# Kernel tuning notes

Hardware: AMD Instinct MI355X
Metric: run time of the kernel (lower is better)

The kernel has to match this reference:

```python
import jax, jax.numpy as jnp
import numpy as np

N_SOTU, N_TAXON = 100000, 20000
E, EL = 800000, 200000
D_S, D_T, H = 256, 128, 256


def setup_inputs() -> dict:
    key = jax.random.key(0)
    ks = jax.random.split(key, 32)
    nrm = lambda k, shp: jax.random.normal(k, shp, jnp.float32) * 0.05
    inp = {}
    inp["x_sotu"] = nrm(ks[0], (N_SOTU, D_S))
    inp["x_taxon"] = nrm(ks[1], (N_TAXON, D_T))
    inp["edge_src"] = jax.random.randint(ks[2], (E,), 0, N_SOTU)   # sotu end
    inp["edge_dst"] = jax.random.randint(ks[3], (E,), 0, N_TAXON)  # taxon end
    inp["label_src"] = jax.random.randint(ks[4], (EL,), 0, N_SOTU)
    inp["label_dst"] = jax.random.randint(ks[5], (EL,), 0, N_TAXON)
    # conv1, edge type sotu->taxon
    inp["Wl1_st"] = nrm(ks[6], (H, D_S)); inp["bl1_st"] = jnp.zeros((H,), jnp.float32)
    inp["Wr1_st"] = nrm(ks[7], (H, D_T))
    # conv1, edge type taxon->sotu (reverse)
    inp["Wl1_ts"] = nrm(ks[8], (H, D_T)); inp["bl1_ts"] = jnp.zeros((H,), jnp.float32)
    inp["Wr1_ts"] = nrm(ks[9], (H, D_S))
    # conv2 (hidden -> hidden) per edge type
    inp["Wl2_st"] = nrm(ks[10], (H, H)); inp["bl2_st"] = jnp.zeros((H,), jnp.float32)
    inp["Wr2_st"] = nrm(ks[11], (H, H))
    inp["Wl2_ts"] = nrm(ks[12], (H, H)); inp["bl2_ts"] = jnp.zeros((H,), jnp.float32)
    inp["Wr2_ts"] = nrm(ks[13], (H, H))
    # final per-node-type linear (to_hetero duplicates Linear per node type)
    inp["Wlin_s"] = nrm(ks[14], (H, H)); inp["blin_s"] = jnp.zeros((H,), jnp.float32)
    inp["Wlin_t"] = nrm(ks[15], (H, H)); inp["blin_t"] = jnp.zeros((H,), jnp.float32)
    # edge decoder MLP
    inp["Wd1"] = nrm(ks[16], (H, 2 * H)); inp["bd1"] = jnp.zeros((H,), jnp.float32)
    inp["Wd2"] = nrm(ks[17], (1, H));     inp["bd2"] = jnp.zeros((1,), jnp.float32)
    return inp


def _sage(x_src, x_dst, src, dst, Wl, bl, Wr):
    """PyG SAGEConv (mean aggr): lin_l(mean of neighbor src feats) + lin_r(x_dst)."""
    n_dst = x_dst.shape[0]
    msum = jax.ops.segment_sum(x_src[src], dst, num_segments=n_dst)
    cnt = jax.ops.segment_sum(jnp.ones(src.shape, x_src.dtype), dst, num_segments=n_dst)
    m = msum / jnp.maximum(cnt, 1.0)[:, None]
    return m @ Wl.T + bl + x_dst @ Wr.T


def reference(x_sotu, x_taxon, edge_src, edge_dst, label_src, label_dst,
              Wl1_st, bl1_st, Wr1_st, Wl1_ts, bl1_ts, Wr1_ts,
              Wl2_st, bl2_st, Wr2_st, Wl2_ts, bl2_ts, Wr2_ts,
              Wlin_s, blin_s, Wlin_t, blin_t, Wd1, bd1, Wd2, bd2):
    # layer 1 (hetero SAGE, aggr='sum' over single incoming edge type per node type)
    h1_t = jax.nn.relu(_sage(x_sotu, x_taxon, edge_src, edge_dst, Wl1_st, bl1_st, Wr1_st))
    h1_s = jax.nn.relu(_sage(x_taxon, x_sotu, edge_dst, edge_src, Wl1_ts, bl1_ts, Wr1_ts))
    # layer 2
    h2_t = jax.nn.relu(_sage(h1_s, h1_t, edge_src, edge_dst, Wl2_st, bl2_st, Wr2_st))
    h2_s = jax.nn.relu(_sage(h1_t, h1_s, edge_dst, edge_src, Wl2_ts, bl2_ts, Wr2_ts))
    # per-node-type output projection
    z_s = h2_s @ Wlin_s.T + blin_s
    z_t = h2_t @ Wlin_t.T + blin_t
    # edge decoder: gather endpoint embeddings, concat, 2-layer MLP
    z = jnp.concatenate([z_s[label_src], z_t[label_dst]], axis=-1)  # [EL, 2H]
    h = jax.nn.relu(z @ Wd1.T + bd1)
    return (h @ Wd2.T + bd2).reshape(-1)  # [EL]
```

## Files before the change

### kernel.cpp

```cpp
#include <hip/hip_runtime.h>


constexpr int NS = 100000, NT = 20000;
constexpr int E_EDGES = 800000, EL_EDGES = 200000;
constexpr int DS = 256, DT = 128, H = 256;

constexpr int NB_T = 79, SH_T = 8, VB_T = 17;
constexpr int NB_S = 98, SH_S = 10, VB_S = 15;
constexpr int BIN_CAP = 96, CHUNK = 2048;
constexpr int CVT_BLOCKS = 2048;

typedef __attribute__((ext_vector_type(8))) short short8;
typedef __attribute__((ext_vector_type(4))) float float4v;
typedef __attribute__((ext_vector_type(8))) _Float16 half8v;
typedef unsigned short ushort_t;

__device__ __forceinline__ float bf2f(unsigned int u) {
    union { unsigned int i; float f; } x; x.i = u << 16; return x.f;
}
__device__ __forceinline__ unsigned short f2bf(float f) {
    union { float f; unsigned int i; } x; x.f = f;
    unsigned int r = x.i + 0x7FFFu + ((x.i >> 16) & 1u);
    return (unsigned short)(r >> 16);
}


struct GemmJob {
    const ushort_t* A1; const ushort_t* W1; int K1;
    const ushort_t* A2; const ushort_t* W2; int K2;
    const ushort_t* Add; const float* bias;
    void* C; int M; int flags;
};

struct GatherJob {
    const ushort_t* X; const int* rowptr; const int* cnt; const int* col;
    ushort_t* out; int N;
};

struct Gather128Job {
    const ushort_t* X; const int* rowptr; const int* cnt; const int* col;
    ushort_t* out; int N;
};

__device__ __forceinline__ void gemm_body(const GemmJob& jb, int bid)
{
    __shared__ ushort_t As[64][40];
    __shared__ ushort_t Bs[128][40];
    const int tid = threadIdx.x;
    const int M = jb.M;

    const int nx = (M + 63) >> 6;
    const int nx8 = nx & ~7;
    int rowblk, colblk;
    if (bid < nx8 * 2) {
        const int group = bid >> 4;
        const int xcd = bid & 7;
        const int half = (bid >> 3) & 1;
        rowblk = group * 8 + xcd;
        colblk = half;
    } else {
        const int r = bid - nx8 * 2;
        rowblk = nx8 + (r >> 1);
        colblk = r & 1;
    }
    const int row0 = rowblk * 64, col0 = colblk * 128;

    const int wave = tid >> 6, lane = tid & 63;
    const int wrow = (wave >> 1) * 32;
    const int wcol = (wave & 1) * 64;
    const int m16 = lane & 15, quad = lane >> 4;
    const int sr = tid >> 2;
    const int skc = (tid & 3) * 8;

    float4v acc[2][4];
#pragma unroll
    for (int i = 0; i < 2; i++)
#pragma unroll
        for (int j = 0; j < 4; j++) acc[i][j] = (float4v){0.f, 0.f, 0.f, 0.f};

#pragma unroll 1
    for (int pass = 0; pass < 2; pass++) {
        const ushort_t* A = pass ? jb.A2 : jb.A1;
        const ushort_t* W = pass ? jb.W2 : jb.W1;
        const int K = pass ? jb.K2 : jb.K1;
        if (!A) break;
        const int gra = row0 + sr;
        const bool oka = gra < M;
        const ushort_t* Ap = A + (size_t)gra * K + skc;
        const ushort_t* Wp0 = W + (size_t)(col0 + sr) * K + skc;
        const ushort_t* Wp1 = W + (size_t)(col0 + 64 + sr) * K + skc;

        uint4 a0 = make_uint4(0, 0, 0, 0);
        if (oka) a0 = *(const uint4*)Ap;
        uint4 b0 = *(const uint4*)Wp0;
        uint4 b1 = *(const uint4*)Wp1;

        for (int k0 = 0; k0 < K; k0 += 32) {
            __syncthreads();
            *(uint4*)&As[sr][skc] = a0;
            *(uint4*)&Bs[sr][skc] = b0;
            *(uint4*)&Bs[64 + sr][skc] = b1;
            __syncthreads();
            if (k0 + 32 < K) {
                a0 = make_uint4(0, 0, 0, 0);
                if (oka) a0 = *(const uint4*)(Ap + k0 + 32);
                b0 = *(const uint4*)(Wp0 + k0 + 32);
                b1 = *(const uint4*)(Wp1 + k0 + 32);
            }
            short8 af[2], bf[4];
#pragma unroll
            for (int i = 0; i < 2; i++)
                af[i] = *(const short8*)&As[wrow + i * 16 + m16][quad * 8];
#pragma unroll
            for (int j = 0; j < 4; j++)
                bf[j] = *(const short8*)&Bs[wcol + j * 16 + m16][quad * 8];
#pragma unroll
            for (int i = 0; i < 2; i++)
#pragma unroll
                for (int j = 0; j < 4; j++)
                    acc[i][j] = __builtin_amdgcn_mfma_f32_16x16x32_bf16(
                        af[i], bf[j], acc[i][j], 0, 0, 0);
        }
    }

    const bool relu = jb.flags & 1, f16out = jb.flags & 2;
#pragma unroll
    for (int i = 0; i < 2; i++) {
        const int rbase = row0 + wrow + i * 16 + quad * 4;
#pragma unroll
        for (int r = 0; r < 4; r++) {
            const int row = rbase + r;
            if (row >= M) continue;
#pragma unroll
            for (int j = 0; j < 4; j++) {
                const int col = col0 + wcol + j * 16 + m16;
                float v = acc[i][j][r];
                if (jb.Add) v += bf2f((unsigned int)jb.Add[(size_t)row * 256 + col]);
                if (jb.bias) v += jb.bias[col];
                if (relu) v = fmaxf(v, 0.f);
                if (f16out) ((_Float16*)jb.C)[(size_t)row * 256 + col] = (_Float16)v;
                else ((ushort_t*)jb.C)[(size_t)row * 256 + col] = f2bf(v);
            }
        }
    }
}

#define UNPACK_ADD(acc, v) \
    acc[0] += bf2f(v.x & 0xffff); acc[1] += bf2f(v.x >> 16); \
    acc[2] += bf2f(v.y & 0xffff); acc[3] += bf2f(v.y >> 16); \
    acc[4] += bf2f(v.z & 0xffff); acc[5] += bf2f(v.z >> 16); \
    acc[6] += bf2f(v.w & 0xffff); acc[7] += bf2f(v.w >> 16);

__device__ __forceinline__ void gather_body(const GatherJob& g, int gb)
{
    const int node = gb * 16 + (threadIdx.x >> 5);
    const int c = (threadIdx.x & 31) * 8;
    if (node >= g.N) return;
    const int beg = g.rowptr[node];
    const int deg = g.cnt[node];
    const int end = beg + deg;
    const ushort_t* __restrict__ X = g.X;
    const int* __restrict__ col = g.col;
    float a[8] = {0, 0, 0, 0, 0, 0, 0, 0};
    float b[8] = {0, 0, 0, 0, 0, 0, 0, 0};
    int i = beg;
    for (; i + 3 < end; i += 4) {
        const int c0 = col[i], c1 = col[i + 1], c2 = col[i + 2], c3 = col[i + 3];
        uint4 v0 = *(const uint4*)&X[(size_t)c0 * 256 + c];
        uint4 v1 = *(const uint4*)&X[(size_t)c1 * 256 + c];
        uint4 v2 = *(const uint4*)&X[(size_t)c2 * 256 + c];
        uint4 v3 = *(const uint4*)&X[(size_t)c3 * 256 + c];
        UNPACK_ADD(a, v0) UNPACK_ADD(b, v1) UNPACK_ADD(a, v2) UNPACK_ADD(b, v3)
    }
    for (; i + 1 < end; i += 2) {
        uint4 v0 = *(const uint4*)&X[(size_t)col[i] * 256 + c];
        uint4 v1 = *(const uint4*)&X[(size_t)col[i + 1] * 256 + c];
        UNPACK_ADD(a, v0) UNPACK_ADD(b, v1)
    }
    if (i < end) {
        uint4 v0 = *(const uint4*)&X[(size_t)col[i] * 256 + c];
        UNPACK_ADD(a, v0)
    }
    float inv = 1.f / fmaxf((float)deg, 1.f);
    uint4 o;
    o.x = (unsigned int)f2bf((a[0] + b[0]) * inv) | ((unsigned int)f2bf((a[1] + b[1]) * inv) << 16);
    o.y = (unsigned int)f2bf((a[2] + b[2]) * inv) | ((unsigned int)f2bf((a[3] + b[3]) * inv) << 16);
    o.z = (unsigned int)f2bf((a[4] + b[4]) * inv) | ((unsigned int)f2bf((a[5] + b[5]) * inv) << 16);
    o.w = (unsigned int)f2bf((a[6] + b[6]) * inv) | ((unsigned int)f2bf((a[7] + b[7]) * inv) << 16);
    *(uint4*)&g.out[(size_t)node * 256 + c] = o;
}

__device__ __forceinline__ void gather128_body(const Gather128Job& g, int gb)
{
    const int node = gb * 32 + (threadIdx.x >> 4);
    const int c = (threadIdx.x & 15) * 8;
    if (node >= g.N) return;
    const int beg = g.rowptr[node];
    const int deg = g.cnt[node];
    const int end = beg + deg;
    const ushort_t* __restrict__ X = g.X;
    const int* __restrict__ col = g.col;
    float a[8] = {0, 0, 0, 0, 0, 0, 0, 0};
    float b[8] = {0, 0, 0, 0, 0, 0, 0, 0};
    int i = beg;
    for (; i + 3 < end; i += 4) {
        const int c0 = col[i], c1 = col[i + 1], c2 = col[i + 2], c3 = col[i + 3];
        uint4 v0 = *(const uint4*)&X[(size_t)c0 * 128 + c];
        uint4 v1 = *(const uint4*)&X[(size_t)c1 * 128 + c];
        uint4 v2 = *(const uint4*)&X[(size_t)c2 * 128 + c];
        uint4 v3 = *(const uint4*)&X[(size_t)c3 * 128 + c];
        UNPACK_ADD(a, v0) UNPACK_ADD(b, v1) UNPACK_ADD(a, v2) UNPACK_ADD(b, v3)
    }
    for (; i + 1 < end; i += 2) {
        uint4 v0 = *(const uint4*)&X[(size_t)col[i] * 128 + c];
        uint4 v1 = *(const uint4*)&X[(size_t)col[i + 1] * 128 + c];
        UNPACK_ADD(a, v0) UNPACK_ADD(b, v1)
    }
    if (i < end) {
        uint4 v0 = *(const uint4*)&X[(size_t)col[i] * 128 + c];
        UNPACK_ADD(a, v0)
    }
    float inv = 1.f / fmaxf((float)deg, 1.f);
    uint4 o;
    o.x = (unsigned int)f2bf((a[0] + b[0]) * inv) | ((unsigned int)f2bf((a[1] + b[1]) * inv) << 16);
    o.y = (unsigned int)f2bf((a[2] + b[2]) * inv) | ((unsigned int)f2bf((a[3] + b[3]) * inv) << 16);
    o.z = (unsigned int)f2bf((a[4] + b[4]) * inv) | ((unsigned int)f2bf((a[5] + b[5]) * inv) << 16);
    o.w = (unsigned int)f2bf((a[6] + b[6]) * inv) | ((unsigned int)f2bf((a[7] + b[7]) * inv) << 16);
    *(uint4*)&g.out[(size_t)node * 128 + c] = o;
}

__device__ __forceinline__ void binA_body(
    const int* __restrict__ key, const int* __restrict__ val, int E,
    int nbins, int shift, int vbits,
    int* __restrict__ gcur, unsigned* __restrict__ stg, int ablk)
{
    __shared__ unsigned bins[NB_S * BIN_CAP];
    __shared__ int lcnt[NB_S], gbase[NB_S];
    const int tid = threadIdx.x;
    const int base = ablk * CHUNK;
    for (int i = tid; i < nbins; i += 256) lcnt[i] = 0;
    __syncthreads();
    const unsigned lowmask = (1u << shift) - 1u;
#pragma unroll
    for (int k = 0; k < CHUNK / 256; k++) {
        int e = base + k * 256 + tid;
        if (e < E) {
            int kk = key[e];
            int b = kk >> shift;
            unsigned pk = (((unsigned)kk & lowmask) << vbits) | (unsigned)val[e];
            int c = atomicAdd(&lcnt[b], 1);
            if (c < BIN_CAP) bins[b * BIN_CAP + c] = pk;
            else { int p = atomicAdd(&gcur[b], 1); stg[p] = pk; }
        }
    }
    __syncthreads();
    if (tid < nbins) gbase[tid] = atomicAdd(&gcur[tid], min(lcnt[tid], BIN_CAP));
    __syncthreads();
    for (int b = 0; b < nbins; b++) {
        int c = min(lcnt[b], BIN_CAP);
        for (int i = tid; i < c; i += 256) stg[gbase[b] + i] = bins[b * BIN_CAP + i];
    }
}

__device__ __forceinline__ void binB_body(
    const unsigned* __restrict__ stg, const int* __restrict__ rowptr,
    int N, int node_per, int vbits, int* __restrict__ colout, int bblk)
{
    __shared__ int cur[1024];
    const int tid = threadIdx.x;
    const int node0 = bblk * node_per;
    const int nn = min(node_per, N - node0);
    for (int i = tid; i < nn; i += 256) cur[i] = rowptr[node0 + i];
    const int estart = rowptr[node0];
    const int eend = rowptr[node0 + nn];
    __syncthreads();
    const unsigned vmask = (1u << vbits) - 1u;
    for (int i = estart + tid; i < eend; i += 256) {
        unsigned v = stg[i];
        int kl = (int)(v >> vbits);
        int pos = atomicAdd(&cur[kl], 1);
        colout[pos] = (int)(v & vmask);
    }
}

struct CvtJobs {
    const float* src[14];
    ushort_t* dst[14];
    int n4[14];
    int cnt;
};

__device__ __forceinline__ void cvt_body(const CvtJobs& jb, int nchunks,
                                         int ch0, int stride)
{
    const int t = threadIdx.x;
#pragma unroll 1
    for (int ch = ch0; ch < nchunks; ch += stride) {
        int idx = ch << 10;
        int k = 0;
        while (idx >= jb.n4[k]) { idx -= jb.n4[k]; ++k; }
        const float4* __restrict__ s = (const float4*)jb.src[k];
        ushort_t* __restrict__ d = jb.dst[k];
        const int base = idx + t;
        float4 v0 = s[base];
        float4 v1 = s[base + 256];
        float4 v2 = s[base + 512];
        float4 v3 = s[base + 768];
        uint2 o0, o1, o2, o3;
        o0.x = (unsigned int)f2bf(v0.x) | ((unsigned int)f2bf(v0.y) << 16);
        o0.y = (unsigned int)f2bf(v0.z) | ((unsigned int)f2bf(v0.w) << 16);
        o1.x = (unsigned int)f2bf(v1.x) | ((unsigned int)f2bf(v1.y) << 16);
        o1.y = (unsigned int)f2bf(v1.z) | ((unsigned int)f2bf(v1.w) << 16);
        o2.x = (unsigned int)f2bf(v2.x) | ((unsigned int)f2bf(v2.y) << 16);
        o2.y = (unsigned int)f2bf(v2.z) | ((unsigned int)f2bf(v2.w) << 16);
        o3.x = (unsigned int)f2bf(v3.x) | ((unsigned int)f2bf(v3.y) << 16);
        o3.y = (unsigned int)f2bf(v3.z) | ((unsigned int)f2bf(v3.w) << 16);
        *(uint2*)(d + (size_t)base * 4) = o0;
        *(uint2*)(d + (size_t)(base + 256) * 4) = o1;
        *(uint2*)(d + (size_t)(base + 512) * 4) = o2;
        *(uint2*)(d + (size_t)(base + 768) * 4) = o3;
    }
}

__device__ __forceinline__ void fold_body(
    const float* __restrict__ Wd1, const float* __restrict__ bd1,
    const float* __restrict__ Wlin_s, const float* __restrict__ blin_s,
    const float* __restrict__ Wlin_t, const float* __restrict__ blin_t,
    float* __restrict__ Wc_s, float* __restrict__ Wc_t,
    float* __restrict__ bu, float* __restrict__ bv, int b)
{
    const int t = threadIdx.x;
    if (b < 256) {
        float s = 0.f;
        for (int k = 0; k < 256; k++) s += Wd1[b * 512 + k] * Wlin_s[k * 256 + t];
        Wc_s[b * 256 + t] = s;
    } else if (b < 512) {
        const int h = b - 256;
        float s = 0.f;
        for (int k = 0; k < 256; k++) s += Wd1[h * 512 + 256 + k] * Wlin_t[k * 256 + t];
        Wc_t[h * 256 + t] = s;
    } else {
        float su = 0.f, sv = 0.f;
        for (int k = 0; k < 256; k++) {
            su += Wd1[t * 512 + k] * blin_s[k];
            sv += Wd1[t * 512 + 256 + k] * blin_t[k];
        }
        bu[t] = bd1[t] + su;
        bv[t] = sv;
    }
}

__device__ __forceinline__ void count_body(
    const int* __restrict__ src, const int* __restrict__ dst,
    int* __restrict__ cnt_s, int* __restrict__ cnt_t, int E, int cblk)
{
    const int base = cblk * 1024 + threadIdx.x;
    const int e0 = base, e1 = base + 256, e2 = base + 512, e3 = base + 768;
    int s0 = 0, s1 = 0, s2 = 0, s3 = 0;
    int d0 = 0, d1 = 0, d2 = 0, d3 = 0;
    if (e0 < E) { s0 = src[e0]; d0 = dst[e0]; }
    if (e1 < E) { s1 = src[e1]; d1 = dst[e1]; }
    if (e2 < E) { s2 = src[e2]; d2 = dst[e2]; }
    if (e3 < E) { s3 = src[e3]; d3 = dst[e3]; }
    if (e0 < E) { atomicAdd(&cnt_s[s0], 1); atomicAdd(&cnt_t[d0], 1); }
    if (e1 < E) { atomicAdd(&cnt_s[s1], 1); atomicAdd(&cnt_t[d1], 1); }
    if (e2 < E) { atomicAdd(&cnt_s[s2], 1); atomicAdd(&cnt_t[d2], 1); }
    if (e3 < E) { atomicAdd(&cnt_s[s3], 1); atomicAdd(&cnt_t[d3], 1); }
}

__global__ __launch_bounds__(256) void gemm_gemm_kernel(GemmJob a, int ablocks,
                                                        GemmJob b)
{
    const int bid = blockIdx.x;
    if (bid < ablocks) gemm_body(a, bid);
    else gemm_body(b, bid - ablocks);
}

__global__ __launch_bounds__(512) void gather_g128_kernel(GatherJob a, int ablocks,
                                                          Gather128Job b)
{
    const int bid = blockIdx.x;
    if (bid < ablocks) gather_body(a, bid);
    else gather128_body(b, bid - ablocks);
}

__global__ __launch_bounds__(512) void gather_gather_kernel(GatherJob a, int ablocks,
                                                            GatherJob b)
{
    const int bid = blockIdx.x;
    if (bid < ablocks) gather_body(a, bid);
    else gather_body(b, bid - ablocks);
}

__global__ __launch_bounds__(256) void fold_count_kernel(
    const float* Wd1, const float* bd1,
    const float* Wlin_s, const float* blin_s,
    const float* Wlin_t, const float* blin_t,
    float* Wc_s, float* Wc_t, float* bu, float* bv,
    const int* src, const int* dst, int* cnt_s, int* cnt_t, int E)
{
    const int bid = blockIdx.x;
    if (bid < 513)
        fold_body(Wd1, bd1, Wlin_s, blin_s, Wlin_t, blin_t, Wc_s, Wc_t, bu, bv, bid);
    else
        count_body(src, dst, cnt_s, cnt_t, E, bid - 513);
}

__global__ __launch_bounds__(256) void cvt_binA_kernel(
    CvtJobs jb, int nchunks, int aBlocks,
    const int* key, const int* val, int E, int nbins, int shift, int vbits,
    int* gcur, unsigned* stg)
{
    const int bid = blockIdx.x;
    if (bid < aBlocks)
        binA_body(key, val, E, nbins, shift, vbits, gcur, stg, bid);
    else
        cvt_body(jb, nchunks, bid - aBlocks, gridDim.x - aBlocks);
}

__global__ __launch_bounds__(256) void binA_binB_kernel(
    const int* keyA, const int* valA, int E, int nbinsA, int shiftA, int vbitsA,
    int* gcurA, unsigned* stgA, int aBlocks,
    const unsigned* stgB, const int* rowptrB, int NB, int nodeperB, int vbitsB,
    int* coloutB)
{
    const int bid = blockIdx.x;
    if (bid < aBlocks)
        binA_body(keyA, valA, E, nbinsA, shiftA, vbitsA, gcurA, stgA, bid);
    else
        binB_body(stgB, rowptrB, NB, nodeperB, vbitsB, coloutB, bid - aBlocks);
}

__global__ __launch_bounds__(256) void binB_kernel(
    const unsigned* __restrict__ stg, const int* __restrict__ rowptr,
    int N, int node_per, int vbits, int* __restrict__ colout)
{
    binB_body(stg, rowptr, N, node_per, vbits, colout, blockIdx.x);
}

__global__ __launch_bounds__(256) void psum_kernel(
    const int* __restrict__ cnt_s, const int* __restrict__ cnt_t,
    int* __restrict__ bsum_s, int* __restrict__ bsum_t, int nbS)
{
    const bool isS = (int)blockIdx.x < nbS;
    const int blk = isS ? blockIdx.x : blockIdx.x - nbS;
    const int N = isS ? NS : NT;
    const int* cnt = isS ? cnt_s : cnt_t;
    int* bsum = isS ? bsum_s : bsum_t;
    __shared__ int sdata[256];
    const int t = threadIdx.x;
    const int base = blk * 1024;
    int s = 0;
    for (int i = t; i < 1024; i += 256) {
        int idx = base + i;
        s += (idx < N) ? cnt[idx] : 0;
    }
    sdata[t] = s; __syncthreads();
    for (int off = 128; off > 0; off >>= 1) {
        if (t < off) sdata[t] += sdata[t + off];
        __syncthreads();
    }
    if (t == 0) bsum[blk] = sdata[0];
}

__global__ void sbsum_kernel(int* __restrict__ bsum_s, int* __restrict__ bsum_t,
                             int nbS, int nbT)
{
    if (threadIdx.x != 0) return;
    int* b = blockIdx.x ? bsum_t : bsum_s;
    int nb = blockIdx.x ? nbT : nbS;
    int run = 0;
    for (int i = 0; i < nb; i++) { int v = b[i]; b[i] = run; run += v; }
}

__global__ __launch_bounds__(256) void sblock_kernel(
    const int* __restrict__ cnt_s, const int* __restrict__ cnt_t,
    const int* __restrict__ bsum_s, const int* __restrict__ bsum_t,
    int* __restrict__ rowptr_s, int* __restrict__ rowptr_t, int nbS)
{
    const bool isS = (int)blockIdx.x < nbS;
    const int blk = isS ? blockIdx.x : blockIdx.x - nbS;
    const int N = isS ? NS : NT;
    const int* cnt = isS ? cnt_s : cnt_t;
    const int* bsum = isS ? bsum_s : bsum_t;
    int* rowptr = isS ? rowptr_s : rowptr_t;
    __shared__ int sc[256];
    const int t = threadIdx.x;
    const int base = blk * 1024 + t * 4;
    int v[4]; int s = 0;
#pragma unroll
    for (int j = 0; j < 4; j++) {
        int idx = base + j;
        v[j] = (idx < N) ? cnt[idx] : 0;
        s += v[j];
    }
    sc[t] = s; __syncthreads();
    for (int off = 1; off < 256; off <<= 1) {
        int add = (t >= off) ? sc[t - off] : 0;
        __syncthreads();
        sc[t] += add;
        __syncthreads();
    }
    int excl = sc[t] - s + bsum[blk];
#pragma unroll
    for (int j = 0; j < 4; j++) {
        int idx = base + j;
        if (idx < N) rowptr[idx] = excl;
        if (idx == N - 1) rowptr[N] = excl + v[j];
        excl += v[j];
    }
}

__global__ void binit_kernel(const int* __restrict__ rowptr_t,
                             const int* __restrict__ rowptr_s,
                             int* __restrict__ gcur_t, int* __restrict__ gcur_s)
{
    int t = threadIdx.x;
    if (t < NB_T) gcur_t[t] = rowptr_t[t << SH_T];
    if (t < NB_S) gcur_s[t] = rowptr_s[t << SH_S];
}

__global__ __launch_bounds__(256) void edge_score_kernel(
    const _Float16* __restrict__ U, const _Float16* __restrict__ V,
    const int* __restrict__ ls, const int* __restrict__ ld,
    const float* __restrict__ Wd2, const float* __restrict__ bd2,
    float* __restrict__ out, int EL)
{
    const int l32 = threadIdx.x & 31;
    const int e = blockIdx.x * 8 + (threadIdx.x >> 5);
    if (e >= EL) return;
    const int c = l32 * 8;
    half8v u = *(const half8v*)&U[(size_t)ls[e] * 256 + c];
    half8v v = *(const half8v*)&V[(size_t)ld[e] * 256 + c];
    float4 w0 = *(const float4*)&Wd2[c];
    float4 w1 = *(const float4*)&Wd2[c + 4];
    float s = fmaxf((float)u[0] + (float)v[0], 0.f) * w0.x
            + fmaxf((float)u[1] + (float)v[1], 0.f) * w0.y
            + fmaxf((float)u[2] + (float)v[2], 0.f) * w0.z
            + fmaxf((float)u[3] + (float)v[3], 0.f) * w0.w
            + fmaxf((float)u[4] + (float)v[4], 0.f) * w1.x
            + fmaxf((float)u[5] + (float)v[5], 0.f) * w1.y
            + fmaxf((float)u[6] + (float)v[6], 0.f) * w1.z
            + fmaxf((float)u[7] + (float)v[7], 0.f) * w1.w;
#pragma unroll
    for (int m = 16; m >= 1; m >>= 1) s += __shfl_xor(s, m, 64);
    if (l32 == 0) out[e] = s + bd2[0];
}

extern "C" void kernel_launch(void* const* d_in, const int* in_sizes, int n_in,
                              void* d_out, int out_size, void* d_ws, size_t ws_size,
                              hipStream_t stream)
{
    const float* x_sotu  = (const float*)d_in[0];
    const float* x_taxon = (const float*)d_in[1];
    const int* edge_src  = (const int*)d_in[2];
    const int* edge_dst  = (const int*)d_in[3];
    const int* label_src = (const int*)d_in[4];
    const int* label_dst = (const int*)d_in[5];
    const float* Wl1_st = (const float*)d_in[6];
    const float* bl1_st = (const float*)d_in[7];
    const float* Wr1_st = (const float*)d_in[8];
    const float* Wl1_ts = (const float*)d_in[9];
    const float* bl1_ts = (const float*)d_in[10];
    const float* Wr1_ts = (const float*)d_in[11];
    const float* Wl2_st = (const float*)d_in[12];
    const float* bl2_st = (const float*)d_in[13];
    const float* Wr2_st = (const float*)d_in[14];
    const float* Wl2_ts = (const float*)d_in[15];
    const float* bl2_ts = (const float*)d_in[16];
    const float* Wr2_ts = (const float*)d_in[17];
    const float* Wlin_s = (const float*)d_in[18];
    const float* blin_s = (const float*)d_in[19];
    const float* Wlin_t = (const float*)d_in[20];
    const float* blin_t = (const float*)d_in[21];
    const float* Wd1 = (const float*)d_in[22];
    const float* bd1 = (const float*)d_in[23];
    const float* Wd2 = (const float*)d_in[24];
    const float* bd2 = (const float*)d_in[25];

    int* wi = (int*)d_ws;
    size_t io = 0;
    int* cnt_s   = wi + io; io += NS;
    int* cnt_t   = wi + io; io += NT;
    int* rowptr_s = wi + io; io += NS + 8;
    int* rowptr_t = wi + io; io += NT + 8;
    int* col_s   = wi + io; io += E_EDGES;
    int* col_t   = wi + io; io += E_EDGES;
    unsigned* stg_s = (unsigned*)(wi + io); io += E_EDGES;
    unsigned* stg_t = (unsigned*)(wi + io); io += E_EDGES;
    int* bsum_s  = wi + io; io += 128;
    int* bsum_t  = wi + io; io += 128;
    int* gcur_t  = wi + io; io += 128;
    int* gcur_s  = wi + io; io += 128;
    io = (io + 63) & ~(size_t)63;

    ushort_t* wb = (ushort_t*)(wi + io);
    size_t bo = 0;
    ushort_t* m_s  = wb + bo; bo += (size_t)NS * H;
    ushort_t* h1_s = wb + bo; bo += (size_t)NS * H;
    ushort_t* m_t  = wb + bo; bo += (size_t)NT * H;
    ushort_t* h1_t = wb + bo; bo += (size_t)NT * H;
    ushort_t* h2_s = wb + bo; bo += (size_t)NS * H;
    ushort_t* h2_t = wb + bo; bo += (size_t)NT * H;
    ushort_t* xs_b = wb + bo; bo += (size_t)NS * DS;
    ushort_t* xt_b = wb + bo; bo += (size_t)NT * DT;
    ushort_t* wb_l1st = wb + bo; bo += H * DS;
    ushort_t* wb_r1st = wb + bo; bo += H * DT;
    ushort_t* wb_l1ts = wb + bo; bo += H * DT;
    ushort_t* wb_r1ts = wb + bo; bo += H * DS;
    ushort_t* wb_l2st = wb + bo; bo += H * H;
    ushort_t* wb_r2st = wb + bo; bo += H * H;
    ushort_t* wb_l2ts = wb + bo; bo += H * H;
    ushort_t* wb_r2ts = wb + bo; bo += H * H;
    ushort_t* wcb_s   = wb + bo; bo += H * H;
    ushort_t* wcb_t   = wb + bo; bo += H * H;
    bo = (bo + 7) & ~(size_t)7;

    float* wf = (float*)(wb + bo);
    size_t fo = 0;
    float* Wc_s = wf + fo; fo += H * H;
    float* Wc_t = wf + fo; fo += H * H;
    float* bu   = wf + fo; fo += 256;
    float* bv   = wf + fo; fo += 256;

    _Float16* U = (_Float16*)m_s;
    _Float16* V = (_Float16*)m_t;

    const dim3 blk(256);
    const dim3 blk512(512);
    auto mgn = [](int M) { return ((M + 63) / 64) * 2; };
    auto g256n = [](int N) { return (N + 15) / 16; };
    auto g128n = [](int N) { return (N + 31) / 32; };
    const int nbS = (NS + 1023) / 1024;
    const int nbT = (NT + 1023) / 1024;
    const int nA = (E_EDGES + CHUNK - 1) / CHUNK;
    const int cntBlocks = (E_EDGES + 1023) / 1024;

    hipMemsetAsync(cnt_s, 0, (size_t)(NS + NT) * sizeof(int), stream);
    fold_count_kernel<<<513 + cntBlocks, blk, 0, stream>>>(
        Wd1, bd1, Wlin_s, blin_s, Wlin_t, blin_t, Wc_s, Wc_t, bu, bv,
        edge_src, edge_dst, cnt_s, cnt_t, E_EDGES);

    psum_kernel<<<nbS + nbT, blk, 0, stream>>>(cnt_s, cnt_t, bsum_s, bsum_t, nbS);
    sbsum_kernel<<<2, 64, 0, stream>>>(bsum_s, bsum_t, nbS, nbT);
    sblock_kernel<<<nbS + nbT, blk, 0, stream>>>(cnt_s, cnt_t, bsum_s, bsum_t,
                                                 rowptr_s, rowptr_t, nbS);
    binit_kernel<<<1, blk, 0, stream>>>(rowptr_t, rowptr_s, gcur_t, gcur_s);

    {
        CvtJobs jb; int c = 0, total4 = 0;
        auto addj = [&](const float* s, ushort_t* d, int n) {
            jb.src[c] = s; jb.dst[c] = d; jb.n4[c] = n / 4; total4 += n / 4; c++;
        };
        addj(x_sotu, xs_b, NS * DS);
        addj(x_taxon, xt_b, NT * DT);
        addj(Wl1_st, wb_l1st, H * DS);
        addj(Wr1_st, wb_r1st, H * DT);
        addj(Wl1_ts, wb_l1ts, H * DT);
        addj(Wr1_ts, wb_r1ts, H * DS);
        addj(Wl2_st, wb_l2st, H * H);
        addj(Wr2_st, wb_r2st, H * H);
        addj(Wl2_ts, wb_l2ts, H * H);
        addj(Wr2_ts, wb_r2ts, H * H);
        addj(Wc_s, wcb_s, H * H);
        addj(Wc_t, wcb_t, H * H);
        jb.cnt = c;
        const int nchunks = total4 >> 10;
        const int cvb = nchunks < CVT_BLOCKS ? nchunks : CVT_BLOCKS;
        cvt_binA_kernel<<<nA + cvb, blk, 0, stream>>>(
            jb, nchunks, nA,
            edge_dst, edge_src, E_EDGES, NB_T, SH_T, VB_T, gcur_t, stg_t);
    }

    binA_binB_kernel<<<nA + NB_T, blk, 0, stream>>>(
        edge_src, edge_dst, E_EDGES, NB_S, SH_S, VB_S, gcur_s, stg_s, nA,
        stg_t, rowptr_t, NT, 1 << SH_T, VB_T, col_t);

    binB_kernel<<<NB_S, blk, 0, stream>>>(stg_s, rowptr_s, NS, 1 << SH_S, VB_S, col_s);

    {
        GatherJob a{xs_b, rowptr_t, cnt_t, col_t, m_t, NT};
        Gather128Job b{xt_b, rowptr_s, cnt_s, col_s, m_s, NS};
        const int ab = g256n(NT);
        gather_g128_kernel<<<ab + g128n(NS), blk512, 0, stream>>>(a, ab, b);
    }
    {
        GemmJob a{xs_b, wb_r1ts, DS, m_s, wb_l1ts, DT, nullptr, bl1_ts, h1_s, NS, 1};
        GemmJob b{m_t, wb_l1st, H, xt_b, wb_r1st, DT, nullptr, bl1_st, h1_t, NT, 1};
        const int ab = mgn(NS);
        gemm_gemm_kernel<<<ab + mgn(NT), blk, 0, stream>>>(a, ab, b);
    }

    {
        GatherJob a{h1_s, rowptr_t, cnt_t, col_t, m_t, NT};
        GatherJob b{h1_t, rowptr_s, cnt_s, col_s, m_s, NS};
        const int ab = g256n(NT);
        gather_gather_kernel<<<ab + g256n(NS), blk512, 0, stream>>>(a, ab, b);
    }
    {
        GemmJob a{h1_s, wb_r2ts, H, m_s, wb_l2ts, H, nullptr, bl2_ts, h2_s, NS, 1};
        GemmJob b{m_t, wb_l2st, H, h1_t, wb_r2st, H, nullptr, bl2_st, h2_t, NT, 1};
        const int ab = mgn(NS);
        gemm_gemm_kernel<<<ab + mgn(NT), blk, 0, stream>>>(a, ab, b);
    }

    {
        GemmJob a{h2_s, wcb_s, H, nullptr, nullptr, 0, nullptr, bu, U, NS, 2};
        GemmJob b{h2_t, wcb_t, H, nullptr, nullptr, 0, nullptr, bv, V, NT, 2};
        const int ab = mgn(NS);
        gemm_gemm_kernel<<<ab + mgn(NT), blk, 0, stream>>>(a, ab, b);
    }
    edge_score_kernel<<<(EL_EDGES + 7) / 8, blk, 0, stream>>>(
        U, V, label_src, label_dst, Wd2, bd2, (float*)d_out, EL_EDGES);
}
```

Measured before the change: 744.3 us.

## Widen GEMM k-step to 64 and fuse binB with taxon gather

The GEMM main loop now stages two 32-wide k slices per iteration in doubled shared-memory buffers, halving the number of barrier pairs and issuing more global loads per step. Separately, the sotu binB pass is launched in the same kernel as the taxon-side gather (which does not depend on it), and the sotu 128-wide gather is split into its own launch afterwards. binB_body now strides by blockDim so it runs correctly with 512 threads. The changes cost more LDS and registers per GEMM block, and binB blocks now carry idle threads.

```diff
diff --git a/kernel.cpp b/kernel.cpp
--- a/kernel.cpp
+++ b/kernel.cpp
@@ -44,8 +44,8 @@
 
 __device__ __forceinline__ void gemm_body(const GemmJob& jb, int bid)
 {
-    __shared__ ushort_t As[64][40];
-    __shared__ ushort_t Bs[128][40];
+    __shared__ ushort_t As[2][64][40];
+    __shared__ ushort_t Bs[2][128][40];
     const int tid = threadIdx.x;
     const int M = jb.M;
 
@@ -90,36 +90,49 @@
         const ushort_t* Wp0 = W + (size_t)(col0 + sr) * K + skc;
         const ushort_t* Wp1 = W + (size_t)(col0 + 64 + sr) * K + skc;
 
-        uint4 a0 = make_uint4(0, 0, 0, 0);
-        if (oka) a0 = *(const uint4*)Ap;
+        uint4 a0 = make_uint4(0, 0, 0, 0), a1 = make_uint4(0, 0, 0, 0);
+        if (oka) { a0 = *(const uint4*)Ap; a1 = *(const uint4*)(Ap + 32); }
         uint4 b0 = *(const uint4*)Wp0;
         uint4 b1 = *(const uint4*)Wp1;
-
-        for (int k0 = 0; k0 < K; k0 += 32) {
+        uint4 b2 = *(const uint4*)(Wp0 + 32);
+        uint4 b3 = *(const uint4*)(Wp1 + 32);
+
+        for (int k0 = 0; k0 < K; k0 += 64) {
             __syncthreads();
-            *(uint4*)&As[sr][skc] = a0;
-            *(uint4*)&Bs[sr][skc] = b0;
-            *(uint4*)&Bs[64 + sr][skc] = b1;
+            *(uint4*)&As[0][sr][skc] = a0;
+            *(uint4*)&As[1][sr][skc] = a1;
+            *(uint4*)&Bs[0][sr][skc] = b0;
+            *(uint4*)&Bs[0][64 + sr][skc] = b1;
+            *(uint4*)&Bs[1][sr][skc] = b2;
+            *(uint4*)&Bs[1][64 + sr][skc] = b3;
             __syncthreads();
-            if (k0 + 32 < K) {
-                a0 = make_uint4(0, 0, 0, 0);
-                if (oka) a0 = *(const uint4*)(Ap + k0 + 32);
-                b0 = *(const uint4*)(Wp0 + k0 + 32);
-                b1 = *(const uint4*)(Wp1 + k0 + 32);
+            if (k0 + 64 < K) {
+                a0 = make_uint4(0, 0, 0, 0); a1 = make_uint4(0, 0, 0, 0);
+                if (oka) {
+                    a0 = *(const uint4*)(Ap + k0 + 64);
+                    a1 = *(const uint4*)(Ap + k0 + 96);
+                }
+                b0 = *(const uint4*)(Wp0 + k0 + 64);
+                b1 = *(const uint4*)(Wp1 + k0 + 64);
+                b2 = *(const uint4*)(Wp0 + k0 + 96);
+                b3 = *(const uint4*)(Wp1 + k0 + 96);
             }
-            short8 af[2], bf[4];
-#pragma unroll
-            for (int i = 0; i < 2; i++)
-                af[i] = *(const short8*)&As[wrow + i * 16 + m16][quad * 8];
-#pragma unroll
-            for (int j = 0; j < 4; j++)
-                bf[j] = *(const short8*)&Bs[wcol + j * 16 + m16][quad * 8];
-#pragma unroll
-            for (int i = 0; i < 2; i++)
+#pragma unroll
+            for (int h = 0; h < 2; h++) {
+                short8 af[2], bf[4];
+#pragma unroll
+                for (int i = 0; i < 2; i++)
+                    af[i] = *(const short8*)&As[h][wrow + i * 16 + m16][quad * 8];
 #pragma unroll
                 for (int j = 0; j < 4; j++)
-                    acc[i][j] = __builtin_amdgcn_mfma_f32_16x16x32_bf16(
-                        af[i], bf[j], acc[i][j], 0, 0, 0);
+                    bf[j] = *(const short8*)&Bs[h][wcol + j * 16 + m16][quad * 8];
+#pragma unroll
+                for (int i = 0; i < 2; i++)
+#pragma unroll
+                    for (int j = 0; j < 4; j++)
+                        acc[i][j] = __builtin_amdgcn_mfma_f32_16x16x32_bf16(
+                            af[i], bf[j], acc[i][j], 0, 0, 0);
+            }
         }
     }
 
@@ -268,14 +281,15 @@
 {
     __shared__ int cur[1024];
     const int tid = threadIdx.x;
+    const int nthr = blockDim.x;
     const int node0 = bblk * node_per;
     const int nn = min(node_per, N - node0);
-    for (int i = tid; i < nn; i += 256) cur[i] = rowptr[node0 + i];
+    for (int i = tid; i < nn; i += nthr) cur[i] = rowptr[node0 + i];
     const int estart = rowptr[node0];
     const int eend = rowptr[node0 + nn];
     __syncthreads();
     const unsigned vmask = (1u << vbits) - 1u;
-    for (int i = estart + tid; i < eend; i += 256) {
+    for (int i = estart + tid; i < eend; i += nthr) {
         unsigned v = stg[i];
         int kl = (int)(v >> vbits);
         int pos = atomicAdd(&cur[kl], 1);
@@ -376,12 +390,9 @@
     else gemm_body(b, bid - ablocks);
 }
 
-__global__ __launch_bounds__(512) void gather_g128_kernel(GatherJob a, int ablocks,
-                                                          Gather128Job b)
-{
-    const int bid = blockIdx.x;
-    if (bid < ablocks) gather_body(a, bid);
-    else gather128_body(b, bid - ablocks);
+__global__ __launch_bounds__(512) void g128_kernel(Gather128Job b)
+{
+    gather128_body(b, blockIdx.x);
 }
 
 __global__ __launch_bounds__(512) void gather_gather_kernel(GatherJob a, int ablocks,
@@ -390,6 +401,15 @@
     const int bid = blockIdx.x;
     if (bid < ablocks) gather_body(a, bid);
     else gather_body(b, bid - ablocks);
+}
+
+__global__ __launch_bounds__(512) void binB_gather_kernel(
+    const unsigned* stg, const int* rowptr, int N, int node_per, int vbits,
+    int* colout, int bBlocks, GatherJob g)
+{
+    const int bid = blockIdx.x;
+    if (bid < bBlocks) binB_body(stg, rowptr, N, node_per, vbits, colout, bid);
+    else gather_body(g, bid - bBlocks);
 }
 
 __global__ __launch_bounds__(256) void fold_count_kernel(
@@ -429,13 +449,6 @@
         binA_body(keyA, valA, E, nbinsA, shiftA, vbitsA, gcurA, stgA, bid);
     else
         binB_body(stgB, rowptrB, NB, nodeperB, vbitsB, coloutB, bid - aBlocks);
-}
-
-__global__ __launch_bounds__(256) void binB_kernel(
-    const unsigned* __restrict__ stg, const int* __restrict__ rowptr,
-    int N, int node_per, int vbits, int* __restrict__ colout)
-{
-    binB_body(stg, rowptr, N, node_per, vbits, colout, blockIdx.x);
 }
 
 __global__ __launch_bounds__(256) void psum_kernel(
@@ -676,14 +689,17 @@
         edge_src, edge_dst, E_EDGES, NB_S, SH_S, VB_S, gcur_s, stg_s, nA,
         stg_t, rowptr_t, NT, 1 << SH_T, VB_T, col_t);
 
-    binB_kernel<<<NB_S, blk, 0, stream>>>(stg_s, rowptr_s, NS, 1 << SH_S, VB_S, col_s);
-
     {
-        GatherJob a{xs_b, rowptr_t, cnt_t, col_t, m_t, NT};
+        GatherJob g{xs_b, rowptr_t, cnt_t, col_t, m_t, NT};
+        binB_gather_kernel<<<NB_S + g256n(NT), blk512, 0, stream>>>(
+            stg_s, rowptr_s, NS, 1 << SH_S, VB_S, col_s, NB_S, g);
+    }
+
+    {
         Gather128Job b{xt_b, rowptr_s, cnt_s, col_s, m_s, NS};
-        const int ab = g256n(NT);
-        gather_g128_kernel<<<ab + g128n(NS), blk512, 0, stream>>>(a, ab, b);
-    }
+        g128_kernel<<<g128n(NS), blk512, 0, stream>>>(b);
+    }
+
     {
         GemmJob a{xs_b, wb_r1ts, DS, m_s, wb_l1ts, DT, nullptr, bl1_ts, h1_s, NS, 1};
         GemmJob b{m_t, wb_l1st, H, xt_b, wb_r1st, DT, nullptr, bl1_st, h1_t, NT, 1};
```

New measurement: 751.4 us. Within noise of the previous version (+1.0%).
